# Optimization experiments

Hardware: AMD Instinct MI355X
Metric: run time of the kernel (lower is better)

## Reference

```python
import jax, jax.numpy as jnp
import numpy as np

B, CLASSES, R, H, W, OUT = 16, 19, 8, 32, 32, 304

def setup_inputs() -> dict:
    key = jax.random.key(0)
    x = jax.random.normal(key, (B, CLASSES * R * R, H, W), dtype=jnp.float32)
    return {"x": x}

def reference(x) -> jnp.ndarray:
    # Depth-to-space (pixel shuffle) matching the torch loop semantics:
    # for each (i,j), x[:, c*r^2:(c+1)*r^2, i, j].reshape(r, r) is written to
    # out[:, c, i*r:(i+1)*r, j*r:(j+1)*r]. Then zero-pad to a fixed 304x304 canvas.
    b = x.shape[0]
    # [b, classes, r, r, H, W]
    t = x.reshape(b, CLASSES, R, R, H, W)
    # -> [b, classes, H, r, W, r] -> [b, classes, H*r, W*r]
    t = jnp.transpose(t, (0, 1, 4, 2, 5, 3)).reshape(b, CLASSES, H * R, W * R)
    pad_h = OUT - H * R  # 304 - 256 = 48 zeros on bottom/right
    pad_w = OUT - W * R
    return jnp.pad(t, ((0, 0), (0, 0), (0, pad_h), (0, pad_w)))
```

## Files before the change

kernel.cpp:

```cpp
#include <hip/hip_runtime.h>


constexpr int B       = 16;
constexpr int CLASSES = 19;
constexpr int H       = 32;
constexpr int W       = 32;
constexpr int OUT     = 304;
constexpr int IN_CH   = CLASSES * 64;
constexpr int OWQ     = OUT / 4;
constexpr int TOTAL_Q = B * CLASSES * OUT * OWQ;

__global__ __launch_bounds__(256) void duc_kernel(const float* __restrict__ x,
                                                  float* __restrict__ out) {
    int tid = blockIdx.x * 256 + threadIdx.x;
    if (tid >= TOTAL_Q) return;

    int owq = tid % OWQ;
    int q   = tid / OWQ;
    int oh  = q % OUT;
    q      /= OUT;
    int c   = q % CLASSES;
    int b   = q / CLASSES;

    int ow0 = owq * 4;

    float4 v = make_float4(0.f, 0.f, 0.f, 0.f);
    if (oh < 256 && ow0 < 256) {
        int i   = oh >> 3;
        int di  = oh & 7;
        int j   = ow0 >> 3;
        int djb = ow0 & 7;
        const float* base = x + (((b * IN_CH + c * 64 + di * 8 + djb) * H + i) * W + j);
        v.x = base[0 * (H * W)];
        v.y = base[1 * (H * W)];
        v.z = base[2 * (H * W)];
        v.w = base[3 * (H * W)];
    }
    reinterpret_cast<float4*>(out)[tid] = v;
}

extern "C" void kernel_launch(void* const* d_in, const int* in_sizes, int n_in,
                              void* d_out, int out_size, void* d_ws, size_t ws_size,
                              hipStream_t stream) {
    const float* x = (const float*)d_in[0];
    float* out     = (float*)d_out;
    int blocks = (TOTAL_Q + 255) / 256;
    duc_kernel<<<blocks, 256, 0, stream>>>(x, out);
}
```

Before: 33.73 us.

## Stage input tiles in LDS for coalesced pixel-shuffle and split padding blocks

Each block now handles one (batch, class, input row): it loads 64 channels × 32 pixels with coalesced float4 reads into padded shared memory, then writes eight output rows as float4 stores by transposing through LDS. Zero padding for the bottom rows goes to dedicated blocks, and the right-edge padding is written by a subset of threads. This replaces the strided scalar gathers of the old version, which touched scattered cache lines, at the cost of a barrier and some LDS bank traffic.

```diff
diff --git a/kernel.cpp b/kernel.cpp
--- a/kernel.cpp
+++ b/kernel.cpp
@@ -7,36 +7,72 @@
 constexpr int W       = 32;
 constexpr int OUT     = 304;
 constexpr int IN_CH   = CLASSES * 64;
+constexpr int HW4     = (H * W) / 4;
 constexpr int OWQ     = OUT / 4;
-constexpr int TOTAL_Q = B * CLASSES * OUT * OWQ;
+constexpr int NB_MAIN = B * CLASSES * H;
+constexpr int PAD_F4  = B * CLASSES * 48 * OWQ;
+constexpr int NB_PAD  = PAD_F4 / 256;
+constexpr int LSTRIDE = 36;
 
 __global__ __launch_bounds__(256) void duc_kernel(const float* __restrict__ x,
                                                   float* __restrict__ out) {
-    int tid = blockIdx.x * 256 + threadIdx.x;
-    if (tid >= TOTAL_Q) return;
+    int t = threadIdx.x;
 
-    int owq = tid % OWQ;
-    int q   = tid / OWQ;
-    int oh  = q % OUT;
-    q      /= OUT;
-    int c   = q % CLASSES;
-    int b   = q / CLASSES;
+    if (blockIdx.x >= NB_MAIN) {
+        int gid = (blockIdx.x - NB_MAIN) * 256 + t;
+        int bc  = gid / (48 * OWQ);
+        int r4  = gid % (48 * OWQ);
+        int pr  = r4 / OWQ;
+        int q   = r4 % OWQ;
+        reinterpret_cast<float4*>(out)[(bc * OUT + 256 + pr) * OWQ + q] =
+            make_float4(0.f, 0.f, 0.f, 0.f);
+        return;
+    }
 
-    int ow0 = owq * 4;
+    __shared__ float lds[64 * LSTRIDE];
 
-    float4 v = make_float4(0.f, 0.f, 0.f, 0.f);
-    if (oh < 256 && ow0 < 256) {
-        int i   = oh >> 3;
-        int di  = oh & 7;
-        int j   = ow0 >> 3;
-        int djb = ow0 & 7;
-        const float* base = x + (((b * IN_CH + c * 64 + di * 8 + djb) * H + i) * W + j);
-        v.x = base[0 * (H * W)];
-        v.y = base[1 * (H * W)];
-        v.z = base[2 * (H * W)];
-        v.w = base[3 * (H * W)];
+    int blk = blockIdx.x;
+    int b   = blk / (CLASSES * H);
+    int rem = blk % (CLASSES * H);
+    int c   = rem / H;
+    int i   = rem % H;
+
+    const float4* x4 = reinterpret_cast<const float4*>(x);
+    int ch0  = t >> 3;
+    int j4i  = t & 7;
+    int gbase = (b * IN_CH + c * 64) * HW4 + i * (W / 4);
+    float4 v0 = x4[gbase + ch0 * HW4 + j4i];
+    float4 v1 = x4[gbase + (ch0 + 32) * HW4 + j4i];
+    *(reinterpret_cast<float4*>(&lds[ch0 * LSTRIDE]) + j4i) = v0;
+    *(reinterpret_cast<float4*>(&lds[(ch0 + 32) * LSTRIDE]) + j4i) = v1;
+    __syncthreads();
+
+    int di = t >> 5;
+    int k  = t & 31;
+    int bc = b * CLASSES + c;
+    int oh = i * 8 + di;
+    float4* orow = reinterpret_cast<float4*>(out) + (bc * OUT + oh) * OWQ;
+
+#pragma unroll
+    for (int s = 0; s < 2; ++s) {
+        int kk  = k + s * 32;
+        int j   = kk >> 1;
+        int djb = (kk & 1) * 4;
+        const float* lrow = &lds[(di * 8 + djb) * LSTRIDE + j];
+        float4 o;
+        o.x = lrow[0 * LSTRIDE];
+        o.y = lrow[1 * LSTRIDE];
+        o.z = lrow[2 * LSTRIDE];
+        o.w = lrow[3 * LSTRIDE];
+        orow[kk] = o;
     }
-    reinterpret_cast<float4*>(out)[tid] = v;
+
+    if (t < 96) {
+        int rowp = t / 12;
+        int cq   = t % 12;
+        reinterpret_cast<float4*>(out)[(bc * OUT + i * 8 + rowp) * OWQ + 64 + cq] =
+            make_float4(0.f, 0.f, 0.f, 0.f);
+    }
 }
 
 extern "C" void kernel_launch(void* const* d_in, const int* in_sizes, int n_in,
@@ -44,6 +80,5 @@
                               hipStream_t stream) {
     const float* x = (const float*)d_in[0];
     float* out     = (float*)d_out;
-    int blocks = (TOTAL_Q + 255) / 256;
-    duc_kernel<<<blocks, 256, 0, stream>>>(x, out);
+    duc_kernel<<<NB_MAIN + NB_PAD, 256, 0, stream>>>(x, out);
 }
```

Result: faster. 32.15 us (-4.7%).
